# Kernel tuning notes

Hardware: AMD Instinct MI355X
Metric: run time of the kernel (lower is better)

The kernel has to match this reference:

```python
import jax, jax.numpy as jnp
import numpy as np

N_BUS = 4096
BATCH = 1024


def setup_inputs() -> dict:
    key = jax.random.key(0)
    ks = jax.random.split(key, 10)
    u = jax.random.normal(ks[0], (BATCH, N_BUS), dtype=jnp.float32)
    w = jax.random.normal(ks[1], (BATCH, N_BUS), dtype=jnp.float32)
    # parameters (torch.rand -> uniform[0,1); Linear init ~ U(-1/sqrt(n), 1/sqrt(n)))
    G = jax.random.uniform(ks[2], (N_BUS, N_BUS), dtype=jnp.float32)
    B = jax.random.uniform(ks[3], (N_BUS, N_BUS), dtype=jnp.float32)
    bias_p = jax.random.uniform(ks[4], (1, N_BUS), dtype=jnp.float32)
    bias_q = jax.random.uniform(ks[5], (1, N_BUS), dtype=jnp.float32)
    lim = 1.0 / np.sqrt(N_BUS)
    Wp = jax.random.uniform(ks[6], (N_BUS, N_BUS), dtype=jnp.float32, minval=-lim, maxval=lim)
    bp = jax.random.uniform(ks[7], (N_BUS,), dtype=jnp.float32, minval=-lim, maxval=lim)
    Wq = jax.random.uniform(ks[8], (N_BUS, N_BUS), dtype=jnp.float32, minval=-lim, maxval=lim)
    bq = jax.random.uniform(ks[9], (N_BUS,), dtype=jnp.float32, minval=-lim, maxval=lim)
    return {"u": u, "w": w, "G": G, "B": B, "bias_p": bias_p, "bias_q": bias_q,
            "Wp": Wp, "bp": bp, "Wq": Wq, "bq": bq}


def reference(u, w, G, B, bias_p, bias_q, Wp, bp, Wq, bq):
    # Algebraically identical to the original's outer-product form:
    # p_i = sum_k (u_i u_k + w_i w_k) G_ik + (w_i u_k - u_i w_k) B_ik
    #     = u_i (G u)_i + w_i (G w)_i + w_i (B u)_i - u_i (B w)_i
    # q_i = sum_k (w_i u_k - u_i w_k) G_ik - (u_i u_k + w_i w_k) B_ik
    #     = w_i (G u)_i - u_i (G w)_i - u_i (B u)_i - w_i (B w)_i
    Gu = u @ G.T  # (batch, n_bus): (G u)_i = sum_k G_ik u_k
    Gw = w @ G.T
    Bu = u @ B.T
    Bw = w @ B.T
    p = u * Gu + w * Gw + w * Bu - u * Bw + bias_p
    q = w * Gu - u * Gw - u * Bu - w * Bw + bias_q
    # nn.Linear: y = x @ W^T + b
    p = p @ Wp.T + bp
    q = q @ Wq.T + bq
    return (p, q)
```

## Files before the change

kernel.cpp:

```cpp
#include <hip/hip_runtime.h>
#include <hip/hip_bf16.h>

#define NB 4096
#define MB 1024
#define SZ ((size_t)MB * NB)
#define NN ((size_t)NB * NB)

typedef __bf16 bf16_t;
typedef __attribute__((ext_vector_type(8))) __bf16 bf16x8;
typedef __attribute__((ext_vector_type(4))) float f32x4;
typedef __attribute__((ext_vector_type(4))) unsigned int u32x4;

__device__ __forceinline__ int swz_off(int r, int kk) {
  return r * 32 + ((kk ^ ((r >> 1) & 3)) << 3);
}

__device__ __forceinline__ bf16x8 neg8(bf16x8 x) {
  u32x4 t;
  __builtin_memcpy(&t, &x, 16);
  t ^= 0x80008000u;
  bf16x8 y;
  __builtin_memcpy(&y, &t, 16);
  return y;
}

__device__ __forceinline__ bf16x8 cvt8(float4 a, float4 b) {
  bf16x8 v;
  v[0] = (bf16_t)a.x; v[1] = (bf16_t)a.y; v[2] = (bf16_t)a.z; v[3] = (bf16_t)a.w;
  v[4] = (bf16_t)b.x; v[5] = (bf16_t)b.y; v[6] = (bf16_t)b.z; v[7] = (bf16_t)b.w;
  return v;
}

#define ITEM_S (SZ / 8)
#define ITEM_N (NN / 8)

__global__ __launch_bounds__(256) void prep6_kernel(
    const float* __restrict__ u, const float* __restrict__ w,
    const float* __restrict__ G, const float* __restrict__ Bm,
    const float* __restrict__ Wp, const float* __restrict__ Wq,
    bf16_t* __restrict__ ws) {
  size_t stride = (size_t)gridDim.x * blockDim.x;
  const size_t tot = 2 * ITEM_S + 4 * ITEM_N;
  for (size_t i = (size_t)blockIdx.x * blockDim.x + threadIdx.x; i < tot;
       i += stride) {
    const float* src;
    bf16_t* dst;
    size_t off;
    if (i < ITEM_S) { src = u; dst = ws; off = i; }
    else if (i < 2 * ITEM_S) { src = w; dst = ws + SZ; off = i - ITEM_S; }
    else if (i < 2 * ITEM_S + ITEM_N) { src = G; dst = ws + 2 * SZ; off = i - 2 * ITEM_S; }
    else if (i < 2 * ITEM_S + 2 * ITEM_N) { src = Bm; dst = ws + 2 * SZ + NN; off = i - 2 * ITEM_S - ITEM_N; }
    else if (i < 2 * ITEM_S + 3 * ITEM_N) { src = Wp; dst = ws + 2 * SZ + 2 * NN; off = i - 2 * ITEM_S - 2 * ITEM_N; }
    else { src = Wq; dst = ws + 2 * SZ + 3 * NN; off = i - 2 * ITEM_S - 3 * ITEM_N; }
    const float4* s = reinterpret_cast<const float4*>(src) + off * 2;
    reinterpret_cast<bf16x8*>(dst)[off] = cvt8(s[0], s[1]);
  }
}

__global__ __launch_bounds__(256) void prep4_kernel(
    const float* __restrict__ u, const float* __restrict__ w,
    const float* __restrict__ G, const float* __restrict__ Bm,
    bf16_t* __restrict__ ws) {
  size_t stride = (size_t)gridDim.x * blockDim.x;
  const size_t tot = 2 * ITEM_S + 2 * ITEM_N;
  for (size_t i = (size_t)blockIdx.x * blockDim.x + threadIdx.x; i < tot;
       i += stride) {
    const float* src;
    bf16_t* dst;
    size_t off;
    if (i < ITEM_S) { src = u; dst = ws; off = i; }
    else if (i < 2 * ITEM_S) { src = w; dst = ws + SZ; off = i - ITEM_S; }
    else if (i < 2 * ITEM_S + ITEM_N) { src = G; dst = ws + 2 * SZ; off = i - 2 * ITEM_S; }
    else { src = Bm; dst = ws + 2 * SZ + NN; off = i - 2 * ITEM_S - ITEM_N; }
    const float4* s = reinterpret_cast<const float4*>(src) + off * 2;
    reinterpret_cast<bf16x8*>(dst)[off] = cvt8(s[0], s[1]);
  }
}

__global__ __launch_bounds__(256, 4) void fused1_v2(
    const float* __restrict__ u, const float* __restrict__ w,
    const bf16_t* __restrict__ ubf, const bf16_t* __restrict__ wbf,
    const bf16_t* __restrict__ Gbf, const bf16_t* __restrict__ Bbf,
    const float* __restrict__ bias_p, const float* __restrict__ bias_q,
    bf16_t* __restrict__ pq) {
  __shared__ bf16_t lds[2][4][64 * 32];
  const int tid = threadIdx.x, lane = tid & 63, wv = tid >> 6;
  const int bid = blockIdx.x;
  const int t = (bid & 7) * 128 + (bid >> 3);
  const int row0 = (t & 15) * 64, col0 = (t >> 4) * 64;
  const int wm = (wv >> 1) * 32, wn = (wv & 1) * 32;
  const int lr = lane & 15, kq = lane >> 4;
  const int fslot = (kq ^ ((lr >> 1) & 3)) << 3;

  const int sr = tid >> 2, skl = tid & 3;
  const int sks = skl ^ ((sr >> 1) & 3);
  const bf16_t* gsrc[4];
  gsrc[0] = ubf + (size_t)(row0 + sr) * NB + (sks << 3);
  gsrc[1] = wbf + (size_t)(row0 + sr) * NB + (sks << 3);
  gsrc[2] = Gbf + (size_t)(col0 + sr) * NB + (sks << 3);
  gsrc[3] = Bbf + (size_t)(col0 + sr) * NB + (sks << 3);
  const int ldsbase = wv * 512;

  f32x4 aS[2][2] = {}, aT[2][2] = {};

#define STAGE1(buf, kt)                                                        \
  {                                                                            \
    _Pragma("unroll") for (int tt = 0; tt < 4; ++tt)                           \
        __builtin_amdgcn_global_load_lds(                                      \
            (const __attribute__((address_space(1))) unsigned int*)(gsrc[tt] + \
                                                                    (kt)),     \
            (__attribute__((address_space(3))) unsigned int*)(&lds[buf][tt]    \
                                                                  [ldsbase]),  \
            16, 0, 0);                                                         \
  }

  STAGE1(0, 0);
  __syncthreads();

  int cur = 0;
  for (int kt = 0; kt < NB; kt += 32) {
    if (kt + 32 < NB) STAGE1(cur ^ 1, kt + 32);
    bf16x8 au[2], aw[2], bG[2], bB[2];
#pragma unroll
    for (int m = 0; m < 2; ++m) {
      int off = (wm + m * 16 + lr) * 32 + fslot;
      au[m] = *reinterpret_cast<const bf16x8*>(&lds[cur][0][off]);
      aw[m] = *reinterpret_cast<const bf16x8*>(&lds[cur][1][off]);
    }
#pragma unroll
    for (int n = 0; n < 2; ++n) {
      int off = (wn + n * 16 + lr) * 32 + fslot;
      bG[n] = *reinterpret_cast<const bf16x8*>(&lds[cur][2][off]);
      bB[n] = *reinterpret_cast<const bf16x8*>(&lds[cur][3][off]);
    }
#pragma unroll
    for (int m = 0; m < 2; ++m)
#pragma unroll
      for (int n = 0; n < 2; ++n) {
        bf16x8 bn = neg8(bB[n]);
        aS[m][n] = __builtin_amdgcn_mfma_f32_16x16x32_bf16(au[m], bG[n], aS[m][n], 0, 0, 0);
        aS[m][n] = __builtin_amdgcn_mfma_f32_16x16x32_bf16(aw[m], bn, aS[m][n], 0, 0, 0);
        aT[m][n] = __builtin_amdgcn_mfma_f32_16x16x32_bf16(aw[m], bG[n], aT[m][n], 0, 0, 0);
        aT[m][n] = __builtin_amdgcn_mfma_f32_16x16x32_bf16(au[m], bB[n], aT[m][n], 0, 0, 0);
      }
    __syncthreads();
    cur ^= 1;
  }

  const int fr = lane & 15, fq = lane >> 4;
#pragma unroll
  for (int m = 0; m < 2; ++m)
#pragma unroll
    for (int n = 0; n < 2; ++n)
#pragma unroll
      for (int j = 0; j < 4; ++j) {
        int r = row0 + wm + m * 16 + fq * 4 + j;
        int c = col0 + wn + n * 16 + fr;
        size_t idx = (size_t)r * NB + c;
        float U = u[idx], W = w[idx];
        float S = aS[m][n][j], T = aT[m][n][j];
        pq[idx] = (bf16_t)(U * S + W * T + bias_p[c]);
        pq[SZ + idx] = (bf16_t)(W * S - U * T + bias_q[c]);
      }
}

__global__ __launch_bounds__(256, 2) void gemm2_v3(
    const bf16_t* __restrict__ pq, const bf16_t* __restrict__ Wpb,
    const bf16_t* __restrict__ Wqb, const float* __restrict__ bp,
    const float* __restrict__ bq, float* __restrict__ out) {
  __shared__ bf16_t lA[2][128 * 32], lW[2][128 * 32];
  const int tid = threadIdx.x, lane = tid & 63, wv = tid >> 6;
  const int bid = blockIdx.x;
  const int t = (bid & 7) * 64 + (bid >> 3);
  const int z = t >> 8;
  const int s = t & 255;
  const int row0 = (s & 7) * 128, col0 = (s >> 3) * 128;

  const bf16_t* A = pq + (size_t)z * SZ;
  const bf16_t* Wm = z ? Wqb : Wpb;
  const float* bias = z ? bq : bp;
  float* C = out + (size_t)z * SZ;

  const int wm = (wv >> 1) * 64, wn = (wv & 1) * 64;
  const int lr = lane & 15, kq = lane >> 4;
  const int fslot = (kq ^ ((lr >> 1) & 3)) << 3;

  f32x4 acc[4][4] = {};

  const bf16_t* gA[2];
  const bf16_t* gW[2];
  int cbase[2];
#pragma unroll
  for (int p = 0; p < 2; ++p) {
    int cb = p * 256 + wv * 64;
    cbase[p] = cb;
    int ci = cb + lane;
    int r = ci >> 2, kl = ci & 3;
    int ks = kl ^ ((r >> 1) & 3);
    gA[p] = A + (size_t)(row0 + r) * NB + (ks << 3);
    gW[p] = Wm + (size_t)(col0 + r) * NB + (ks << 3);
  }

#define STAGE2(buf, kt)                                                        \
  {                                                                            \
    _Pragma("unroll") for (int p = 0; p < 2; ++p) {                            \
      __builtin_amdgcn_global_load_lds(                                        \
          (const __attribute__((address_space(1))) unsigned int*)(gA[p] +      \
                                                                  (kt)),       \
          (__attribute__((address_space(3))) unsigned int*)(&lA[buf]           \
                                                               [cbase[p] * 8]),\
          16, 0, 0);                                                           \
      __builtin_amdgcn_global_load_lds(                                        \
          (const __attribute__((address_space(1))) unsigned int*)(gW[p] +      \
                                                                  (kt)),       \
          (__attribute__((address_space(3))) unsigned int*)(&lW[buf]           \
                                                               [cbase[p] * 8]),\
          16, 0, 0);                                                           \
    }                                                                          \
  }

  STAGE2(0, 0);
  __syncthreads();

  int cur = 0;
  for (int kt = 0; kt < NB; kt += 32) {
    if (kt + 32 < NB) STAGE2(cur ^ 1, kt + 32);
    bf16x8 af[4], bg[4];
#pragma unroll
    for (int m = 0; m < 4; ++m)
      af[m] = *reinterpret_cast<const bf16x8*>(&lA[cur][(wm + m * 16 + lr) * 32 + fslot]);
#pragma unroll
    for (int n = 0; n < 4; ++n)
      bg[n] = *reinterpret_cast<const bf16x8*>(&lW[cur][(wn + n * 16 + lr) * 32 + fslot]);
#pragma unroll
    for (int m = 0; m < 4; ++m)
#pragma unroll
      for (int n = 0; n < 4; ++n)
        acc[m][n] = __builtin_amdgcn_mfma_f32_16x16x32_bf16(af[m], bg[n], acc[m][n], 0, 0, 0);
    __syncthreads();
    cur ^= 1;
  }

  const int fr = lane & 15, fq = lane >> 4;
#pragma unroll
  for (int m = 0; m < 4; ++m)
#pragma unroll
    for (int n = 0; n < 4; ++n)
#pragma unroll
      for (int j = 0; j < 4; ++j) {
        int r = row0 + wm + m * 16 + fq * 4 + j;
        int c = col0 + wn + n * 16 + fr;
        C[(size_t)r * NB + c] = acc[m][n][j] + bias[c];
      }
}

__device__ __forceinline__ void fb_stage_f32(const float* __restrict__ src,
                                             int row0, int k0, bf16_t* lds, int t) {
  int r = t >> 2, kk = t & 3;
  const float* p = src + (size_t)(row0 + r) * NB + k0 + (kk << 3);
  float4 v0 = *reinterpret_cast<const float4*>(p);
  float4 v1 = *reinterpret_cast<const float4*>(p + 4);
  *reinterpret_cast<bf16x8*>(lds + swz_off(r, kk)) = cvt8(v0, v1);
}

__global__ __launch_bounds__(256, 2) void fb_gemm2(
    const bf16_t* __restrict__ pq, const float* __restrict__ Wp,
    const float* __restrict__ Wq, const float* __restrict__ bp,
    const float* __restrict__ bq, float* __restrict__ out) {
  __shared__ bf16_t lA[128 * 32], lW[128 * 32];
  const int z = blockIdx.z;
  const bf16_t* A = pq + (size_t)z * SZ;
  const float* Wm = z ? Wq : Wp;
  const float* bias = z ? bq : bp;
  float* C = out + (size_t)z * SZ;
  const int tid = threadIdx.x;
  const int lane = tid & 63, wv = tid >> 6;
  const int wm = (wv >> 1) * 64, wn = (wv & 1) * 64;
  const int row0 = blockIdx.y * 128, col0 = blockIdx.x * 128;
  const int lr = lane & 15, kq = lane >> 4;
  const int fslot = (kq ^ ((lr >> 1) & 3)) << 3;
  f32x4 acc[4][4] = {};
  for (int kt = 0; kt < NB; kt += 32) {
#pragma unroll
    for (int p = 0; p < 2; ++p) {
      int cb = p * 256 + wv * 64;
      int ci = cb + lane;
      int r = ci >> 2, kl = ci & 3;
      int ks = kl ^ ((r >> 1) & 3);
      const bf16_t* g = A + (size_t)(row0 + r) * NB + kt + (ks << 3);
      __builtin_amdgcn_global_load_lds(
          (const __attribute__((address_space(1))) unsigned int*)g,
          (__attribute__((address_space(3))) unsigned int*)(lA + cb * 8),
          16, 0, 0);
    }
#pragma unroll
    for (int p = 0; p < 2; ++p)
      fb_stage_f32(Wm, col0, kt, lW, p * 256 + tid);
    __syncthreads();
    bf16x8 af[4], bg[4];
#pragma unroll
    for (int m = 0; m < 4; ++m)
      af[m] = *reinterpret_cast<const bf16x8*>(lA + (wm + m * 16 + lr) * 32 + fslot);
#pragma unroll
    for (int n = 0; n < 4; ++n)
      bg[n] = *reinterpret_cast<const bf16x8*>(lW + (wn + n * 16 + lr) * 32 + fslot);
#pragma unroll
    for (int m = 0; m < 4; ++m)
#pragma unroll
      for (int n = 0; n < 4; ++n)
        acc[m][n] = __builtin_amdgcn_mfma_f32_16x16x32_bf16(af[m], bg[n], acc[m][n], 0, 0, 0);
    __syncthreads();
  }
  const int fr = lane & 15, fq = lane >> 4;
#pragma unroll
  for (int m = 0; m < 4; ++m)
#pragma unroll
    for (int n = 0; n < 4; ++n)
#pragma unroll
      for (int j = 0; j < 4; ++j) {
        int r = row0 + wm + m * 16 + fq * 4 + j;
        int c = col0 + wn + n * 16 + fr;
        C[(size_t)r * NB + c] = acc[m][n][j] + bias[c];
      }
}

__global__ __launch_bounds__(512, 2) void fb_fused1(
    const float* __restrict__ u, const float* __restrict__ w,
    const float* __restrict__ G, const float* __restrict__ Bm,
    const float* __restrict__ bias_p, const float* __restrict__ bias_q,
    bf16_t* __restrict__ pq) {
  __shared__ bf16_t lU[128 * 32], lW[128 * 32], lG[128 * 32], lB[128 * 32];
  const int tid = threadIdx.x;
  const int lane = tid & 63, wv = tid >> 6;
  const int wm = (wv >> 2) * 64, wn = (wv & 3) * 32;
  const int row0 = blockIdx.y * 128, col0 = blockIdx.x * 128;
  const int lr = lane & 15, kq = lane >> 4;
  const int fslot = (kq ^ ((lr >> 1) & 3)) << 3;
  f32x4 aS[4][2] = {}, aT[4][2] = {};
  for (int kt = 0; kt < NB; kt += 32) {
    fb_stage_f32(u, row0, kt, lU, tid);
    fb_stage_f32(w, row0, kt, lW, tid);
    fb_stage_f32(G, col0, kt, lG, tid);
    fb_stage_f32(Bm, col0, kt, lB, tid);
    __syncthreads();
    bf16x8 au[4], aw[4], bG[2], bB[2], bBn[2];
#pragma unroll
    for (int m = 0; m < 4; ++m) {
      int off = (wm + m * 16 + lr) * 32 + fslot;
      au[m] = *reinterpret_cast<const bf16x8*>(lU + off);
      aw[m] = *reinterpret_cast<const bf16x8*>(lW + off);
    }
#pragma unroll
    for (int n = 0; n < 2; ++n) {
      int off = (wn + n * 16 + lr) * 32 + fslot;
      bG[n] = *reinterpret_cast<const bf16x8*>(lG + off);
      bB[n] = *reinterpret_cast<const bf16x8*>(lB + off);
      bBn[n] = neg8(bB[n]);
    }
#pragma unroll
    for (int m = 0; m < 4; ++m)
#pragma unroll
      for (int n = 0; n < 2; ++n) {
        aS[m][n] = __builtin_amdgcn_mfma_f32_16x16x32_bf16(au[m], bG[n], aS[m][n], 0, 0, 0);
        aS[m][n] = __builtin_amdgcn_mfma_f32_16x16x32_bf16(aw[m], bBn[n], aS[m][n], 0, 0, 0);
        aT[m][n] = __builtin_amdgcn_mfma_f32_16x16x32_bf16(aw[m], bG[n], aT[m][n], 0, 0, 0);
        aT[m][n] = __builtin_amdgcn_mfma_f32_16x16x32_bf16(au[m], bB[n], aT[m][n], 0, 0, 0);
      }
    __syncthreads();
  }
  const int fr = lane & 15, fq = lane >> 4;
#pragma unroll
  for (int m = 0; m < 4; ++m)
#pragma unroll
    for (int n = 0; n < 2; ++n)
#pragma unroll
      for (int j = 0; j < 4; ++j) {
        int r = row0 + wm + m * 16 + fq * 4 + j;
        int c = col0 + wn + n * 16 + fr;
        size_t idx = (size_t)r * NB + c;
        float U = u[idx], W = w[idx];
        float S = aS[m][n][j], T = aT[m][n][j];
        pq[idx] = (bf16_t)(U * S + W * T + bias_p[c]);
        pq[SZ + idx] = (bf16_t)(W * S - U * T + bias_q[c]);
      }
}

extern "C" void kernel_launch(void* const* d_in, const int* in_sizes, int n_in,
                              void* d_out, int out_size, void* d_ws, size_t ws_size,
                              hipStream_t stream) {
  const float* u = (const float*)d_in[0];
  const float* w = (const float*)d_in[1];
  const float* G = (const float*)d_in[2];
  const float* Bm = (const float*)d_in[3];
  const float* bias_p = (const float*)d_in[4];
  const float* bias_q = (const float*)d_in[5];
  const float* Wp = (const float*)d_in[6];
  const float* bp = (const float*)d_in[7];
  const float* Wq = (const float*)d_in[8];
  const float* bq = (const float*)d_in[9];
  (void)in_sizes; (void)n_in; (void)out_size;

  const size_t need_full = (4 * SZ + 4 * NN) * sizeof(bf16_t);
  const size_t need_mid = (4 * SZ + 2 * NN) * sizeof(bf16_t);

  if (ws_size >= need_full) {
    bf16_t* ws = (bf16_t*)d_ws;
    bf16_t* ubf = ws;
    bf16_t* wbf = ws + SZ;
    bf16_t* Gbf = ws + 2 * SZ;
    bf16_t* Bbf = Gbf + NN;
    bf16_t* Wpb = Bbf + NN;
    bf16_t* Wqb = Wpb + NN;
    bf16_t* pqw = Wqb + NN;
    prep6_kernel<<<2048, 256, 0, stream>>>(u, w, G, Bm, Wp, Wq, ws);
    fused1_v2<<<1024, 256, 0, stream>>>(u, w, ubf, wbf, Gbf, Bbf,
                                        bias_p, bias_q, pqw);
    gemm2_v3<<<512, 256, 0, stream>>>(pqw, Wpb, Wqb, bp, bq, (float*)d_out);
  } else if (ws_size >= need_mid) {
    bf16_t* ws = (bf16_t*)d_ws;
    bf16_t* ubf = ws;
    bf16_t* wbf = ws + SZ;
    bf16_t* Gbf = ws + 2 * SZ;
    bf16_t* Bbf = Gbf + NN;
    bf16_t* pqw = Bbf + NN;
    prep4_kernel<<<2048, 256, 0, stream>>>(u, w, G, Bm, ws);
    fused1_v2<<<1024, 256, 0, stream>>>(u, w, ubf, wbf, Gbf, Bbf,
                                        bias_p, bias_q, pqw);
    fb_gemm2<<<dim3(NB / 128, MB / 128, 2), 256, 0, stream>>>(
        pqw, Wp, Wq, bp, bq, (float*)d_out);
  } else {
    bf16_t* pqw = (bf16_t*)d_ws;
    fb_fused1<<<dim3(NB / 128, MB / 128), 512, 0, stream>>>(
        u, w, G, Bm, bias_p, bias_q, pqw);
    fb_gemm2<<<dim3(NB / 128, MB / 128, 2), 256, 0, stream>>>(
        pqw, Wp, Wq, bp, bq, (float*)d_out);
  }
}
```

Before: 369.9 us.

## Enlarge GEMM tiles to 8-wave blocks with BK=64 and interleaved prefetch

```diff
diff --git a/kernel.cpp b/kernel.cpp
--- a/kernel.cpp
+++ b/kernel.cpp
@@ -11,9 +11,9 @@
 typedef __attribute__((ext_vector_type(4))) float f32x4;
 typedef __attribute__((ext_vector_type(4))) unsigned int u32x4;
 
-__device__ __forceinline__ int swz_off(int r, int kk) {
-  return r * 32 + ((kk ^ ((r >> 1) & 3)) << 3);
-}
+#define AS1 __attribute__((address_space(1)))
+#define AS3 __attribute__((address_space(3)))
+
 
 __device__ __forceinline__ bf16x8 neg8(bf16x8 x) {
   u32x4 t;
@@ -30,6 +30,8 @@
   v[4] = (bf16_t)b.x; v[5] = (bf16_t)b.y; v[6] = (bf16_t)b.z; v[7] = (bf16_t)b.w;
   return v;
 }
+
+#define MFMA16(a, b, c) __builtin_amdgcn_mfma_f32_16x16x32_bf16((a), (b), (c), 0, 0, 0)
 
 #define ITEM_S (SZ / 8)
 #define ITEM_N (NN / 8)
@@ -77,79 +79,117 @@
   }
 }
 
-__global__ __launch_bounds__(256, 4) void fused1_v2(
+__global__ __launch_bounds__(512, 2) void fused1_v3(
     const float* __restrict__ u, const float* __restrict__ w,
     const bf16_t* __restrict__ ubf, const bf16_t* __restrict__ wbf,
     const bf16_t* __restrict__ Gbf, const bf16_t* __restrict__ Bbf,
     const float* __restrict__ bias_p, const float* __restrict__ bias_q,
     bf16_t* __restrict__ pq) {
-  __shared__ bf16_t lds[2][4][64 * 32];
+  __shared__ bf16_t lds[2][4][128 * 64];
   const int tid = threadIdx.x, lane = tid & 63, wv = tid >> 6;
   const int bid = blockIdx.x;
-  const int t = (bid & 7) * 128 + (bid >> 3);
-  const int row0 = (t & 15) * 64, col0 = (t >> 4) * 64;
-  const int wm = (wv >> 1) * 32, wn = (wv & 1) * 32;
+  const int t = (bid & 7) * 32 + (bid >> 3);
+  const int row0 = (t & 7) * 128, col0 = (t >> 3) * 128;
+  const int wm = (wv >> 2) * 64, wn = (wv & 3) * 32;
   const int lr = lane & 15, kq = lane >> 4;
-  const int fslot = (kq ^ ((lr >> 1) & 3)) << 3;
-
-  const int sr = tid >> 2, skl = tid & 3;
-  const int sks = skl ^ ((sr >> 1) & 3);
-  const bf16_t* gsrc[4];
-  gsrc[0] = ubf + (size_t)(row0 + sr) * NB + (sks << 3);
-  gsrc[1] = wbf + (size_t)(row0 + sr) * NB + (sks << 3);
-  gsrc[2] = Gbf + (size_t)(col0 + sr) * NB + (sks << 3);
-  gsrc[3] = Bbf + (size_t)(col0 + sr) * NB + (sks << 3);
-  const int ldsbase = wv * 512;
-
-  f32x4 aS[2][2] = {}, aT[2][2] = {};
-
-#define STAGE1(buf, kt)                                                        \
-  {                                                                            \
-    _Pragma("unroll") for (int tt = 0; tt < 4; ++tt)                           \
-        __builtin_amdgcn_global_load_lds(                                      \
-            (const __attribute__((address_space(1))) unsigned int*)(gsrc[tt] + \
-                                                                    (kt)),     \
-            (__attribute__((address_space(3))) unsigned int*)(&lds[buf][tt]    \
-                                                                  [ldsbase]),  \
-            16, 0, 0);                                                         \
-  }
-
-  STAGE1(0, 0);
+
+  const int rA = tid >> 3;
+  const int kkc = (tid & 7) ^ (rA & 7);
+  const bf16_t* bases[4] = {ubf, wbf, Gbf, Bbf};
+  const int r0s[4] = {row0, row0, col0, col0};
+  const bf16_t* gsA[4];
+  const bf16_t* gsB[4];
+#pragma unroll
+  for (int o = 0; o < 4; ++o) {
+    gsA[o] = bases[o] + (size_t)(r0s[o] + rA) * NB + kkc * 8;
+    gsB[o] = gsA[o] + (size_t)64 * NB;
+  }
+
+#define F1_ST(bufv, o, ktn)                                                    \
+  do {                                                                         \
+    __builtin_amdgcn_global_load_lds(                                          \
+        (const AS1 unsigned int*)(gsA[o] + (ktn)),                             \
+        (AS3 unsigned int*)(&lds[bufv][o][wv * 512]), 16, 0, 0);               \
+    __builtin_amdgcn_global_load_lds(                                          \
+        (const AS1 unsigned int*)(gsB[o] + (ktn)),                             \
+        (AS3 unsigned int*)(&lds[bufv][o][4096 + wv * 512]), 16, 0, 0);        \
+  } while (0)
+
+  int kread[2], aoff[4], boff[2];
+#pragma unroll
+  for (int ks = 0; ks < 2; ++ks) kread[ks] = ((ks * 4 + kq) ^ (lr & 7)) << 3;
+#pragma unroll
+  for (int m = 0; m < 4; ++m) aoff[m] = (wm + m * 16 + lr) * 64;
+#pragma unroll
+  for (int n = 0; n < 2; ++n) boff[n] = (wn + n * 16 + lr) * 64;
+
+#define F1_LD(o, roff, ks) \
+  (*reinterpret_cast<const bf16x8*>(&lds[cur][o][(roff) + kread[ks]]))
+
+  f32x4 aS[4][2] = {}, aT[4][2] = {};
+
+  {
+    F1_ST(0, 0, 0); F1_ST(0, 1, 0); F1_ST(0, 2, 0); F1_ST(0, 3, 0);
+    asm volatile("s_waitcnt vmcnt(0)" ::: "memory");
+  }
   __syncthreads();
 
-  int cur = 0;
-  for (int kt = 0; kt < NB; kt += 32) {
-    if (kt + 32 < NB) STAGE1(cur ^ 1, kt + 32);
-    bf16x8 au[2], aw[2], bG[2], bB[2];
-#pragma unroll
-    for (int m = 0; m < 2; ++m) {
-      int off = (wm + m * 16 + lr) * 32 + fslot;
-      au[m] = *reinterpret_cast<const bf16x8*>(&lds[cur][0][off]);
-      aw[m] = *reinterpret_cast<const bf16x8*>(&lds[cur][1][off]);
+  const int NIT = NB / 64;
+  for (int it = 0; it < NIT; ++it) {
+    const int cur = it & 1;
+    const int nxt = cur ^ 1;
+    const bool pf = (it + 1) < NIT;
+    const int ktn = (it + 1) * 64;
+#pragma unroll
+    for (int ks = 0; ks < 2; ++ks) {
+      bf16x8 bG[2], bB[2], bBn[2];
+#pragma unroll
+      for (int mh = 0; mh < 2; ++mh) {
+        if (mh == 0) {
+          bG[0] = F1_LD(2, boff[0], ks);
+          bG[1] = F1_LD(2, boff[1], ks);
+          bB[0] = F1_LD(3, boff[0], ks);
+          bB[1] = F1_LD(3, boff[1], ks);
+          bBn[0] = neg8(bB[0]);
+          bBn[1] = neg8(bB[1]);
+        }
+        bf16x8 au2[2], aw2[2];
+#pragma unroll
+        for (int i = 0; i < 2; ++i) {
+          au2[i] = F1_LD(0, aoff[2 * mh + i], ks);
+          aw2[i] = F1_LD(1, aoff[2 * mh + i], ks);
+        }
+        if (ks == 0 && pf) {
+          if (mh == 0) { F1_ST(nxt, 0, ktn); F1_ST(nxt, 1, ktn); }
+          else         { F1_ST(nxt, 2, ktn); F1_ST(nxt, 3, ktn); }
+        }
+        __builtin_amdgcn_s_barrier();
+        __builtin_amdgcn_sched_barrier(0);
+        __builtin_amdgcn_s_setprio(1);
+#pragma unroll
+        for (int i = 0; i < 2; ++i) {
+          const int m = 2 * mh + i;
+#pragma unroll
+          for (int n = 0; n < 2; ++n) {
+            aS[m][n] = MFMA16(au2[i], bG[n], aS[m][n]);
+            aS[m][n] = MFMA16(aw2[i], bBn[n], aS[m][n]);
+            aT[m][n] = MFMA16(aw2[i], bG[n], aT[m][n]);
+            aT[m][n] = MFMA16(au2[i], bB[n], aT[m][n]);
+          }
+        }
+        __builtin_amdgcn_s_setprio(0);
+        __builtin_amdgcn_sched_barrier(0);
+        if (ks == 1 && mh == 1)
+          asm volatile("s_waitcnt vmcnt(0)" ::: "memory");
+        __builtin_amdgcn_s_barrier();
+        __builtin_amdgcn_sched_barrier(0);
+      }
     }
-#pragma unroll
-    for (int n = 0; n < 2; ++n) {
-      int off = (wn + n * 16 + lr) * 32 + fslot;
-      bG[n] = *reinterpret_cast<const bf16x8*>(&lds[cur][2][off]);
-      bB[n] = *reinterpret_cast<const bf16x8*>(&lds[cur][3][off]);
-    }
-#pragma unroll
-    for (int m = 0; m < 2; ++m)
-#pragma unroll
-      for (int n = 0; n < 2; ++n) {
-        bf16x8 bn = neg8(bB[n]);
-        aS[m][n] = __builtin_amdgcn_mfma_f32_16x16x32_bf16(au[m], bG[n], aS[m][n], 0, 0, 0);
-        aS[m][n] = __builtin_amdgcn_mfma_f32_16x16x32_bf16(aw[m], bn, aS[m][n], 0, 0, 0);
-        aT[m][n] = __builtin_amdgcn_mfma_f32_16x16x32_bf16(aw[m], bG[n], aT[m][n], 0, 0, 0);
-        aT[m][n] = __builtin_amdgcn_mfma_f32_16x16x32_bf16(au[m], bB[n], aT[m][n], 0, 0, 0);
-      }
-    __syncthreads();
-    cur ^= 1;
-  }
-
-  const int fr = lane & 15, fq = lane >> 4;
-#pragma unroll
-  for (int m = 0; m < 2; ++m)
+  }
+
+  const int fr = lane & 15, fq = kq;
+#pragma unroll
+  for (int m = 0; m < 4; ++m)
 #pragma unroll
     for (int n = 0; n < 2; ++n)
 #pragma unroll
@@ -164,84 +204,113 @@
       }
 }
 
-__global__ __launch_bounds__(256, 2) void gemm2_v3(
+__global__ __launch_bounds__(512, 2) void gemm2_v4(
     const bf16_t* __restrict__ pq, const bf16_t* __restrict__ Wpb,
     const bf16_t* __restrict__ Wqb, const float* __restrict__ bp,
     const float* __restrict__ bq, float* __restrict__ out) {
-  __shared__ bf16_t lA[2][128 * 32], lW[2][128 * 32];
+  __shared__ bf16_t lA[2][128 * 64];
+  __shared__ bf16_t lW[2][256 * 64];
   const int tid = threadIdx.x, lane = tid & 63, wv = tid >> 6;
   const int bid = blockIdx.x;
-  const int t = (bid & 7) * 64 + (bid >> 3);
-  const int z = t >> 8;
-  const int s = t & 255;
-  const int row0 = (s & 7) * 128, col0 = (s >> 3) * 128;
+  const int t = (bid & 7) * 32 + (bid >> 3);
+  const int z = t >> 7;
+  const int s = t & 127;
+  const int row0 = (s & 7) * 128, col0 = (s >> 3) * 256;
 
   const bf16_t* A = pq + (size_t)z * SZ;
   const bf16_t* Wm = z ? Wqb : Wpb;
   const float* bias = z ? bq : bp;
   float* C = out + (size_t)z * SZ;
 
-  const int wm = (wv >> 1) * 64, wn = (wv & 1) * 64;
+  const int wm = (wv >> 2) * 64, wn = (wv & 3) * 64;
   const int lr = lane & 15, kq = lane >> 4;
-  const int fslot = (kq ^ ((lr >> 1) & 3)) << 3;
+
+  const int rA = tid >> 3;
+  const int kkc = (tid & 7) ^ (rA & 7);
+  const bf16_t* gA_[2];
+  const bf16_t* gW_[4];
+#pragma unroll
+  for (int j = 0; j < 2; ++j)
+    gA_[j] = A + (size_t)(row0 + rA + 64 * j) * NB + kkc * 8;
+#pragma unroll
+  for (int j = 0; j < 4; ++j)
+    gW_[j] = Wm + (size_t)(col0 + rA + 64 * j) * NB + kkc * 8;
+
+#define G2_STA(bufv, j, ktn)                                                   \
+  __builtin_amdgcn_global_load_lds(                                            \
+      (const AS1 unsigned int*)(gA_[j] + (ktn)),                               \
+      (AS3 unsigned int*)(&lA[bufv][(j) * 4096 + wv * 512]), 16, 0, 0)
+#define G2_STW(bufv, j, ktn)                                                   \
+  __builtin_amdgcn_global_load_lds(                                            \
+      (const AS1 unsigned int*)(gW_[j] + (ktn)),                               \
+      (AS3 unsigned int*)(&lW[bufv][(j) * 4096 + wv * 512]), 16, 0, 0)
+
+  int kread[2], aoff[4], boff[4];
+#pragma unroll
+  for (int ks = 0; ks < 2; ++ks) kread[ks] = ((ks * 4 + kq) ^ (lr & 7)) << 3;
+#pragma unroll
+  for (int m = 0; m < 4; ++m) aoff[m] = (wm + m * 16 + lr) * 64;
+#pragma unroll
+  for (int n = 0; n < 4; ++n) boff[n] = (wn + n * 16 + lr) * 64;
 
   f32x4 acc[4][4] = {};
 
-  const bf16_t* gA[2];
-  const bf16_t* gW[2];
-  int cbase[2];
-#pragma unroll
-  for (int p = 0; p < 2; ++p) {
-    int cb = p * 256 + wv * 64;
-    cbase[p] = cb;
-    int ci = cb + lane;
-    int r = ci >> 2, kl = ci & 3;
-    int ks = kl ^ ((r >> 1) & 3);
-    gA[p] = A + (size_t)(row0 + r) * NB + (ks << 3);
-    gW[p] = Wm + (size_t)(col0 + r) * NB + (ks << 3);
-  }
-
-#define STAGE2(buf, kt)                                                        \
-  {                                                                            \
-    _Pragma("unroll") for (int p = 0; p < 2; ++p) {                            \
-      __builtin_amdgcn_global_load_lds(                                        \
-          (const __attribute__((address_space(1))) unsigned int*)(gA[p] +      \
-                                                                  (kt)),       \
-          (__attribute__((address_space(3))) unsigned int*)(&lA[buf]           \
-                                                               [cbase[p] * 8]),\
-          16, 0, 0);                                                           \
-      __builtin_amdgcn_global_load_lds(                                        \
-          (const __attribute__((address_space(1))) unsigned int*)(gW[p] +      \
-                                                                  (kt)),       \
-          (__attribute__((address_space(3))) unsigned int*)(&lW[buf]           \
-                                                               [cbase[p] * 8]),\
-          16, 0, 0);                                                           \
-    }                                                                          \
-  }
-
-  STAGE2(0, 0);
+  {
+    G2_STA(0, 0, 0); G2_STA(0, 1, 0);
+    G2_STW(0, 0, 0); G2_STW(0, 1, 0); G2_STW(0, 2, 0); G2_STW(0, 3, 0);
+    asm volatile("s_waitcnt vmcnt(0)" ::: "memory");
+  }
   __syncthreads();
 
-  int cur = 0;
-  for (int kt = 0; kt < NB; kt += 32) {
-    if (kt + 32 < NB) STAGE2(cur ^ 1, kt + 32);
-    bf16x8 af[4], bg[4];
-#pragma unroll
-    for (int m = 0; m < 4; ++m)
-      af[m] = *reinterpret_cast<const bf16x8*>(&lA[cur][(wm + m * 16 + lr) * 32 + fslot]);
-#pragma unroll
-    for (int n = 0; n < 4; ++n)
-      bg[n] = *reinterpret_cast<const bf16x8*>(&lW[cur][(wn + n * 16 + lr) * 32 + fslot]);
-#pragma unroll
-    for (int m = 0; m < 4; ++m)
-#pragma unroll
-      for (int n = 0; n < 4; ++n)
-        acc[m][n] = __builtin_amdgcn_mfma_f32_16x16x32_bf16(af[m], bg[n], acc[m][n], 0, 0, 0);
-    __syncthreads();
-    cur ^= 1;
-  }
-
-  const int fr = lane & 15, fq = lane >> 4;
+  const int NIT = NB / 64;
+  for (int it = 0; it < NIT; ++it) {
+    const int cur = it & 1;
+    const int nxt = cur ^ 1;
+    const bool pf = (it + 1) < NIT;
+    const int ktn = (it + 1) * 64;
+#pragma unroll
+    for (int ks = 0; ks < 2; ++ks) {
+      bf16x8 bw[4];
+#pragma unroll
+      for (int mh = 0; mh < 2; ++mh) {
+        if (mh == 0) {
+#pragma unroll
+          for (int n = 0; n < 4; ++n)
+            bw[n] = *reinterpret_cast<const bf16x8*>(
+                &lW[cur][boff[n] + kread[ks]]);
+        }
+        bf16x8 au2[2];
+#pragma unroll
+        for (int i = 0; i < 2; ++i)
+          au2[i] = *reinterpret_cast<const bf16x8*>(
+              &lA[cur][aoff[2 * mh + i] + kread[ks]]);
+        if (pf) {
+          const int ph = ks * 2 + mh;
+          if (ph == 0) { G2_STA(nxt, 0, ktn); G2_STA(nxt, 1, ktn); }
+          else if (ph == 1) { G2_STW(nxt, 0, ktn); G2_STW(nxt, 1, ktn); }
+          else if (ph == 2) { G2_STW(nxt, 2, ktn); G2_STW(nxt, 3, ktn); }
+        }
+        __builtin_amdgcn_s_barrier();
+        __builtin_amdgcn_sched_barrier(0);
+        __builtin_amdgcn_s_setprio(1);
+#pragma unroll
+        for (int i = 0; i < 2; ++i) {
+          const int m = 2 * mh + i;
+#pragma unroll
+          for (int n = 0; n < 4; ++n)
+            acc[m][n] = MFMA16(au2[i], bw[n], acc[m][n]);
+        }
+        __builtin_amdgcn_s_setprio(0);
+        __builtin_amdgcn_sched_barrier(0);
+        if (ks == 1 && mh == 1)
+          asm volatile("s_waitcnt vmcnt(0)" ::: "memory");
+        __builtin_amdgcn_s_barrier();
+        __builtin_amdgcn_sched_barrier(0);
+      }
+    }
+  }
+
+  const int fr = lane & 15, fq = kq;
 #pragma unroll
   for (int m = 0; m < 4; ++m)
 #pragma unroll
@@ -252,6 +321,10 @@
         int c = col0 + wn + n * 16 + fr;
         C[(size_t)r * NB + c] = acc[m][n][j] + bias[c];
       }
+}
+
+__device__ __forceinline__ int swz_off32(int r, int kk) {
+  return r * 32 + ((kk ^ ((r >> 1) & 3)) << 3);
 }
 
 __device__ __forceinline__ void fb_stage_f32(const float* __restrict__ src,
@@ -260,7 +333,7 @@
   const float* p = src + (size_t)(row0 + r) * NB + k0 + (kk << 3);
   float4 v0 = *reinterpret_cast<const float4*>(p);
   float4 v1 = *reinterpret_cast<const float4*>(p + 4);
-  *reinterpret_cast<bf16x8*>(lds + swz_off(r, kk)) = cvt8(v0, v1);
+  *reinterpret_cast<bf16x8*>(lds + swz_off32(r, kk)) = cvt8(v0, v1);
 }
 
 __global__ __launch_bounds__(256, 2) void fb_gemm2(
@@ -288,10 +361,8 @@
       int r = ci >> 2, kl = ci & 3;
       int ks = kl ^ ((r >> 1) & 3);
       const bf16_t* g = A + (size_t)(row0 + r) * NB + kt + (ks << 3);
-      __builtin_amdgcn_global_load_lds(
-          (const __attribute__((address_space(1))) unsigned int*)g,
-          (__attribute__((address_space(3))) unsigned int*)(lA + cb * 8),
-          16, 0, 0);
+      __builtin_amdgcn_global_load_lds((const AS1 unsigned int*)g,
+                                       (AS3 unsigned int*)(lA + cb * 8), 16, 0, 0);
     }
 #pragma unroll
     for (int p = 0; p < 2; ++p)
@@ -308,7 +379,7 @@
     for (int m = 0; m < 4; ++m)
 #pragma unroll
       for (int n = 0; n < 4; ++n)
-        acc[m][n] = __builtin_amdgcn_mfma_f32_16x16x32_bf16(af[m], bg[n], acc[m][n], 0, 0, 0);
+        acc[m][n] = MFMA16(af[m], bg[n], acc[m][n]);
     __syncthreads();
   }
   const int fr = lane & 15, fq = lane >> 4;
@@ -361,10 +432,10 @@
     for (int m = 0; m < 4; ++m)
 #pragma unroll
       for (int n = 0; n < 2; ++n) {
-        aS[m][n] = __builtin_amdgcn_mfma_f32_16x16x32_bf16(au[m], bG[n], aS[m][n], 0, 0, 0);
-        aS[m][n] = __builtin_amdgcn_mfma_f32_16x16x32_bf16(aw[m], bBn[n], aS[m][n], 0, 0, 0);
-        aT[m][n] = __builtin_amdgcn_mfma_f32_16x16x32_bf16(aw[m], bG[n], aT[m][n], 0, 0, 0);
-        aT[m][n] = __builtin_amdgcn_mfma_f32_16x16x32_bf16(au[m], bB[n], aT[m][n], 0, 0, 0);
+        aS[m][n] = MFMA16(au[m], bG[n], aS[m][n]);
+        aS[m][n] = MFMA16(aw[m], bBn[n], aS[m][n]);
+        aT[m][n] = MFMA16(aw[m], bG[n], aT[m][n]);
+        aT[m][n] = MFMA16(au[m], bB[n], aT[m][n]);
       }
     __syncthreads();
   }
@@ -400,8 +471,8 @@
   const float* bq = (const float*)d_in[9];
   (void)in_sizes; (void)n_in; (void)out_size;
 
-  const size_t need_full = (4 * SZ + 4 * NN) * sizeof(bf16_t);
-  const size_t need_mid = (4 * SZ + 2 * NN) * sizeof(bf16_t);
+  const size_t need_full = (6 * SZ + 4 * NN) * sizeof(bf16_t);
+  const size_t need_mid = (6 * SZ + 2 * NN) * sizeof(bf16_t);
 
   if (ws_size >= need_full) {
     bf16_t* ws = (bf16_t*)d_ws;
@@ -413,9 +484,9 @@
     bf16_t* Wqb = Wpb + NN;
     bf16_t* pqw = Wqb + NN;
     prep6_kernel<<<2048, 256, 0, stream>>>(u, w, G, Bm, Wp, Wq, ws);
-    fused1_v2<<<1024, 256, 0, stream>>>(u, w, ubf, wbf, Gbf, Bbf,
-                                        bias_p, bias_q, pqw);
-    gemm2_v3<<<512, 256, 0, stream>>>(pqw, Wpb, Wqb, bp, bq, (float*)d_out);
+    fused1_v3<<<256, 512, 0, stream>>>(u, w, ubf, wbf, Gbf, Bbf,
+                                       bias_p, bias_q, pqw);
+    gemm2_v4<<<256, 512, 0, stream>>>(pqw, Wpb, Wqb, bp, bq, (float*)d_out);
   } else if (ws_size >= need_mid) {
     bf16_t* ws = (bf16_t*)d_ws;
     bf16_t* ubf = ws;
@@ -424,8 +495,8 @@
     bf16_t* Bbf = Gbf + NN;
     bf16_t* pqw = Bbf + NN;
     prep4_kernel<<<2048, 256, 0, stream>>>(u, w, G, Bm, ws);
-    fused1_v2<<<1024, 256, 0, stream>>>(u, w, ubf, wbf, Gbf, Bbf,
-                                        bias_p, bias_q, pqw);
+    fused1_v3<<<256, 512, 0, stream>>>(u, w, ubf, wbf, Gbf, Bbf,
+                                       bias_p, bias_q, pqw);
     fb_gemm2<<<dim3(NB / 128, MB / 128, 2), 256, 0, stream>>>(
         pqw, Wp, Wq, bp, bq, (float*)d_out);
   } else {
```

Result: faster. 340.8 us (-7.9%).
